# Optimization experiments

Hardware: AMD Instinct MI355X
Metric: run time of the kernel (lower is better)

The kernel has to match this reference:

```python
import jax, jax.numpy as jnp
import numpy as np

N_NODES = 100000
N_EDGES = 6400000
NUM_FEATURES = 128
NUM_CLASSES = 4


def _gcn_conv(x, W, b, src, dst, n):
    # PyG GCNConv: h = x @ W, symmetric norm over edges (self-loops already added),
    # scatter-add messages to dst, then add bias.
    h = x @ W                                            # [N, out]
    deg = jax.ops.segment_sum(jnp.ones(dst.shape[0], x.dtype), dst, num_segments=n)
    dinv = jnp.where(deg > 0, jax.lax.rsqrt(deg), 0.0)   # deg^-1/2, 0 for isolated
    norm = dinv[src] * dinv[dst]                         # [E]
    agg = jax.ops.segment_sum(h[src] * norm[:, None], dst, num_segments=n)
    return agg + b


def setup_inputs() -> dict:
    key = jax.random.key(0)
    ks = jax.random.split(key, 10)
    x = jax.random.normal(ks[0], (N_NODES, NUM_FEATURES), dtype=jnp.float32)
    edge_index = jax.random.randint(ks[1], (2, N_EDGES), 0, N_NODES, dtype=jnp.int32)

    def lin(k, fan_in, fan_out):
        s = 1.0 / np.sqrt(fan_in)
        return jax.random.uniform(k, (fan_in, fan_out), jnp.float32, -s, s)

    return {
        "x": x,
        "edge_index": edge_index,
        "W1": lin(ks[2], NUM_FEATURES, 4), "b1": jnp.zeros((4,), jnp.float32),
        "W2": lin(ks[3], 4, 4),            "b2": jnp.zeros((4,), jnp.float32),
        "W3": lin(ks[4], 4, 2),            "b3": jnp.zeros((2,), jnp.float32),
        "Wc": lin(ks[5], 2, NUM_CLASSES),  "bc": jnp.zeros((NUM_CLASSES,), jnp.float32),
    }


def reference(x, edge_index, W1, b1, W2, b2, W3, b3, Wc, bc):
    n = x.shape[0]
    loops = jnp.arange(n, dtype=edge_index.dtype)
    src = jnp.concatenate([edge_index[0], loops])  # add self-loops once; graph fixed across layers
    dst = jnp.concatenate([edge_index[1], loops])

    h = jnp.tanh(_gcn_conv(x, W1, b1, src, dst, n))
    h = jnp.tanh(_gcn_conv(h, W2, b2, src, dst, n))
    h = jnp.tanh(_gcn_conv(h, W3, b3, src, dst, n))
    out = h @ Wc + bc
    return (out, h)
```

## Files before the change

### kernel.cpp

```cpp
#include <hip/hip_runtime.h>
#include <math.h>


#define LCHUNK 16384
#define CHUNK2 16000
#define MAXNB  512
#define CAP    18432
#define MAXNB2 1024
#define CAP2   9600

__device__ __forceinline__ int swz_chunk(int bid, int G) {
    if ((G & 7) != 0) return bid;
    return (bid & 7) * (G >> 3) + (bid >> 3);
}

__global__ __launch_bounds__(1024) void k_local(
        const int* __restrict__ src, const int* __restrict__ dst,
        int* __restrict__ packed, int* __restrict__ hbT, int* __restrict__ loff,
        int NBK, int G, int e) {
    __shared__ int hist[MAXNB];
    __shared__ int cur[MAXNB];
    __shared__ int part[1024];
    __shared__ int stage[LCHUNK];
    int g = blockIdx.x, tid = threadIdx.x;
    for (int b = tid; b < NBK; b += 1024) hist[b] = 0;
    __syncthreads();
    int i0 = g * LCHUNK;
    int i1 = min(i0 + LCHUNK, e);
    int val[16], bkt[16];
#pragma unroll
    for (int k = 0; k < 16; k++) {
        int i = i0 + tid + (k << 10);
        bool v = i < i1;
        int d = v ? dst[i] : 0;
        int s = v ? src[i] : 0;
        bkt[k] = v ? (d >> 8) : -1;
        val[k] = ((d & 255) << 17) | s;
        if (v) atomicAdd(&hist[d >> 8], 1);
    }
    __syncthreads();
    int s0 = (tid < NBK) ? hist[tid] : 0;
    part[tid] = s0;
    __syncthreads();
#pragma unroll
    for (int off = 1; off < 1024; off <<= 1) {
        int u = (tid >= off) ? part[tid - off] : 0;
        __syncthreads();
        part[tid] += u;
        __syncthreads();
    }
    int excl = part[tid] - s0;
    if (tid < NBK) {
        cur[tid] = excl;
        hbT[(size_t)tid * G + g] = s0;
        loff[(size_t)g * NBK + tid] = excl;
    }
    __syncthreads();
#pragma unroll
    for (int k = 0; k < 16; k++) {
        if (bkt[k] >= 0) {
            int p = atomicAdd(&cur[bkt[k]], 1);
            stage[p] = val[k];
        }
    }
    __syncthreads();
    int len = i1 - i0;
    for (int i = tid; i < len; i += 1024)
        packed[i0 + i] = stage[i];
}

__global__ void k_scanA(int* __restrict__ hbT, int* __restrict__ btot, int G) {
    __shared__ int part[256];
    int b = blockIdx.x, t = threadIdx.x;
    int* row = hbT + (size_t)b * G;
    int C = (G + 255) / 256;
    int lo = t * C, hi = min(lo + C, G);
    int s = 0;
    for (int i = lo; i < hi; i++) s += row[i];
    part[t] = s;
    __syncthreads();
#pragma unroll
    for (int off = 1; off < 256; off <<= 1) {
        int u = (t >= off) ? part[t - off] : 0;
        __syncthreads();
        part[t] += u;
        __syncthreads();
    }
    int run = part[t] - s;
    for (int i = lo; i < hi; i++) {
        int v = row[i];
        row[i] = run;
        run += v;
    }
    if (t == 255) btot[b] = part[255];
}

__global__ void k_scanB(const int* __restrict__ btot, int* __restrict__ bstart,
                        int NB, int e) {
    __shared__ int part[512];
    int t = threadIdx.x;
    int C = (NB + 511) / 512;
    int lo = t * C, hi = min(lo + C, NB);
    int s = 0;
    for (int i = lo; i < hi; i++) s += btot[i];
    part[t] = s;
    __syncthreads();
#pragma unroll
    for (int off = 1; off < 512; off <<= 1) {
        int u = (t >= off) ? part[t - off] : 0;
        __syncthreads();
        part[t] += u;
        __syncthreads();
    }
    int run = part[t] - s;
    for (int i = lo; i < hi; i++) {
        bstart[i] = run;
        run += btot[i];
    }
    if (t == 511) bstart[NB] = e;
}

__global__ __launch_bounds__(512) void k_merge(
        const int* __restrict__ hbT, const int* __restrict__ loff,
        const int* __restrict__ btot, const int* __restrict__ bstart,
        const int* __restrict__ packed, int* __restrict__ csr,
        float* __restrict__ dinv, int* __restrict__ rowoff,
        int NBK, int G, int n) {
    __shared__ int stage[CAP];
    __shared__ int stage2[CAP];
    __shared__ int cnt[256];
    __shared__ int off[256];
    __shared__ int cur[256];
    int b = blockIdx.x, tid = threadIdx.x;
    int btt = btot[b];
    int total = min(btt, CAP);
    for (int g = tid; g < G; g += 512) {
        int o  = hbT[(size_t)b * G + g];
        int nx = (g + 1 < G) ? hbT[(size_t)b * G + g + 1] : btt;
        if (nx > CAP) nx = CAP;
        if (o >= nx) continue;
        int len = nx - o;
        int sp = g * LCHUNK + loff[(size_t)g * NBK + b];
        int a   = sp & ~3;
        int rel = sp - a;
        int n4  = (rel + len + 3) >> 2;
        for (int q = 0; q < n4; q++) {
            int4 w = *reinterpret_cast<const int4*>(packed + a + q * 4);
            int base = q * 4 - rel;
            if (base >= 0 && base < len)     stage[o + base]     = w.x;
            if (base + 1 >= 0 && base + 1 < len) stage[o + base + 1] = w.y;
            if (base + 2 >= 0 && base + 2 < len) stage[o + base + 2] = w.z;
            if (base + 3 >= 0 && base + 3 < len) stage[o + base + 3] = w.w;
        }
    }
    if (tid < 256) cnt[tid] = 0;
    __syncthreads();
    for (int i = tid; i < total; i += 512) atomicAdd(&cnt[stage[i] >> 17], 1);
    __syncthreads();
    if (tid < 256) off[tid] = cnt[tid];
    __syncthreads();
#pragma unroll
    for (int s = 1; s < 256; s <<= 1) {
        int v = 0;
        if (tid < 256 && tid >= s) v = off[tid - s];
        __syncthreads();
        if (tid < 256 && tid >= s) off[tid] += v;
        __syncthreads();
    }
    if (tid < 256) {
        int excl = off[tid] - cnt[tid];
        int node = (b << 8) + tid;
        if (node < n) dinv[node] = 1.0f / sqrtf((float)(cnt[tid] + 1));
        if (node <= n) rowoff[node] = bstart[b] + excl;
        cur[tid] = excl;
    }
    __syncthreads();
    for (int i = tid; i < total; i += 512) {
        int w = stage[i];
        int p = atomicAdd(&cur[w >> 17], 1);
        stage2[p] = w & 0x1FFFF;
    }
    __syncthreads();
    int base = bstart[b];
    for (int i = tid; i < total; i += 512)
        csr[base + i] = stage2[i];
}

__global__ void k_hist_o(const int* __restrict__ dst, int* __restrict__ hbT,
                         int NB, int G, int e) {
    __shared__ int hist[MAXNB2];
    int g = swz_chunk(blockIdx.x, G);
    for (int b = threadIdx.x; b < NB; b += 512) hist[b] = 0;
    __syncthreads();
    long long i0 = (long long)g * CHUNK2;
    int i1 = (int)min(i0 + CHUNK2, (long long)e);
    for (int i = (int)i0 + threadIdx.x; i < i1; i += 512)
        atomicAdd(&hist[dst[i] >> 7], 1);
    __syncthreads();
    for (int b = threadIdx.x; b < NB; b += 512)
        hbT[(size_t)b * G + g] = hist[b];
}

__global__ void k_part_o(const int* __restrict__ src, const int* __restrict__ dst,
                         const int* __restrict__ hbT, const int* __restrict__ bstart,
                         int* __restrict__ packed, int NB, int G, int e) {
    __shared__ int cur[MAXNB2];
    int g = swz_chunk(blockIdx.x, G);
    for (int b = threadIdx.x; b < NB; b += 512)
        cur[b] = hbT[(size_t)b * G + g] + bstart[b];
    __syncthreads();
    long long i0 = (long long)g * CHUNK2;
    int i1 = (int)min(i0 + CHUNK2, (long long)e);
    for (int i = (int)i0 + threadIdx.x; i < i1; i += 512) {
        int d = dst[i], s = src[i];
        int pos = atomicAdd(&cur[d >> 7], 1);
        packed[pos] = ((d & 127) << 17) | s;
    }
}

__global__ void k_build_o(const int* __restrict__ bstart, int* __restrict__ packed,
                          float* __restrict__ dinv, int* __restrict__ rowoff, int n) {
    __shared__ int stage[CAP2];
    __shared__ int cnt[128];
    __shared__ int off[128];
    __shared__ int cur[128];
    int b = blockIdx.x, tid = threadIdx.x;
    int lo = bstart[b];
    int len = bstart[b + 1] - lo;
    if (len > CAP2) len = CAP2;
    if (tid < 128) cnt[tid] = 0;
    for (int i = tid; i < len; i += 256) stage[i] = packed[lo + i];
    __syncthreads();
    for (int i = tid; i < len; i += 256) atomicAdd(&cnt[stage[i] >> 17], 1);
    __syncthreads();
    if (tid < 128) off[tid] = cnt[tid];
    __syncthreads();
#pragma unroll
    for (int s = 1; s < 128; s <<= 1) {
        int v = 0;
        if (tid < 128 && tid >= s) v = off[tid - s];
        __syncthreads();
        if (tid < 128 && tid >= s) off[tid] += v;
        __syncthreads();
    }
    if (tid < 128) {
        int excl = off[tid] - cnt[tid];
        int node = (b << 7) + tid;
        if (node < n) dinv[node] = 1.0f / sqrtf((float)(cnt[tid] + 1));
        if (node <= n) rowoff[node] = lo + excl;
        cur[tid] = excl;
    }
    __syncthreads();
    for (int i = tid; i < len; i += 256) {
        int w = stage[i];
        int p = atomicAdd(&cur[w >> 17], 1);
        packed[lo + p] = w & 0x1FFFF;
    }
}

__global__ void k_mm1(const float* __restrict__ x, const float* __restrict__ W,
                      const float* __restrict__ dinv, float* __restrict__ hs, int n) {
    int gid = blockIdx.x * blockDim.x + threadIdx.x;
    int node = gid >> 6;
    int lane = threadIdx.x & 63;
    if (node >= n) return;
    const float2 xv = *reinterpret_cast<const float2*>(x + (size_t)node * 128 + lane * 2);
    const float4 w0 = *reinterpret_cast<const float4*>(W + (lane * 2) * 4);
    const float4 w1 = *reinterpret_cast<const float4*>(W + (lane * 2 + 1) * 4);
    float a0 = xv.x * w0.x + xv.y * w1.x;
    float a1 = xv.x * w0.y + xv.y * w1.y;
    float a2 = xv.x * w0.z + xv.y * w1.z;
    float a3 = xv.x * w0.w + xv.y * w1.w;
#pragma unroll
    for (int m = 32; m >= 1; m >>= 1) {
        a0 += __shfl_xor(a0, m);
        a1 += __shfl_xor(a1, m);
        a2 += __shfl_xor(a2, m);
        a3 += __shfl_xor(a3, m);
    }
    if (lane == 0) {
        float di = dinv[node];
        *reinterpret_cast<float4*>(hs + (size_t)node * 4) =
            make_float4(a0 * di, a1 * di, a2 * di, a3 * di);
    }
}

template <int FOUT>
__global__ void k_gath_fin4(const int* __restrict__ rowoff, const int* __restrict__ csr,
                            const float* __restrict__ hs, const float* __restrict__ dinv,
                            const float* __restrict__ b, const float* __restrict__ Wn,
                            float* __restrict__ hsn, int n) {
    int gid = blockIdx.x * blockDim.x + threadIdx.x;
    int node = gid >> 6;
    int lane = threadIdx.x & 63;
    if (node >= n) return;
    int start = rowoff[node], end = rowoff[node + 1];
    float a0 = 0.f, a1 = 0.f, a2 = 0.f, a3 = 0.f;
    for (int j = start + lane; j < end; j += 64) {
        int s = csr[j];
        float4 v = *reinterpret_cast<const float4*>(hs + (size_t)s * 4);
        a0 += v.x; a1 += v.y; a2 += v.z; a3 += v.w;
    }
#pragma unroll
    for (int m = 32; m >= 1; m >>= 1) {
        a0 += __shfl_xor(a0, m);
        a1 += __shfl_xor(a1, m);
        a2 += __shfl_xor(a2, m);
        a3 += __shfl_xor(a3, m);
    }
    if (lane == 0) {
        float4 s = *reinterpret_cast<const float4*>(hs + (size_t)node * 4);
        float di = dinv[node];
        float h0 = tanhf((a0 + s.x) * di + b[0]);
        float h1 = tanhf((a1 + s.y) * di + b[1]);
        float h2 = tanhf((a2 + s.z) * di + b[2]);
        float h3 = tanhf((a3 + s.w) * di + b[3]);
        float o[FOUT];
#pragma unroll
        for (int j = 0; j < FOUT; j++) {
            o[j] = (h0 * Wn[0 * FOUT + j] + h1 * Wn[1 * FOUT + j] +
                    h2 * Wn[2 * FOUT + j] + h3 * Wn[3 * FOUT + j]) * di;
        }
        if constexpr (FOUT == 4) {
            *reinterpret_cast<float4*>(hsn + (size_t)node * 4) =
                make_float4(o[0], o[1], o[2], o[3]);
        } else {
            *reinterpret_cast<float2*>(hsn + (size_t)node * 2) = make_float2(o[0], o[1]);
        }
    }
}

__global__ void k_gath_fin3(const int* __restrict__ rowoff, const int* __restrict__ csr,
                            const float* __restrict__ hs, const float* __restrict__ dinv,
                            const float* __restrict__ b3, const float* __restrict__ Wc,
                            const float* __restrict__ bc, float* __restrict__ out,
                            float* __restrict__ hout, int n) {
    int gid = blockIdx.x * blockDim.x + threadIdx.x;
    int node = gid >> 6;
    int lane = threadIdx.x & 63;
    if (node >= n) return;
    int start = rowoff[node], end = rowoff[node + 1];
    float a0 = 0.f, a1 = 0.f;
    for (int j = start + lane; j < end; j += 64) {
        int s = csr[j];
        float2 v = *reinterpret_cast<const float2*>(hs + (size_t)s * 2);
        a0 += v.x; a1 += v.y;
    }
#pragma unroll
    for (int m = 32; m >= 1; m >>= 1) {
        a0 += __shfl_xor(a0, m);
        a1 += __shfl_xor(a1, m);
    }
    if (lane == 0) {
        float2 s = *reinterpret_cast<const float2*>(hs + (size_t)node * 2);
        float di = dinv[node];
        float h0 = tanhf((a0 + s.x) * di + b3[0]);
        float h1 = tanhf((a1 + s.y) * di + b3[1]);
        *reinterpret_cast<float2*>(hout + (size_t)node * 2) = make_float2(h0, h1);
        float4 o;
        o.x = h0 * Wc[0] + h1 * Wc[4] + bc[0];
        o.y = h0 * Wc[1] + h1 * Wc[5] + bc[1];
        o.z = h0 * Wc[2] + h1 * Wc[6] + bc[2];
        o.w = h0 * Wc[3] + h1 * Wc[7] + bc[3];
        *reinterpret_cast<float4*>(out + (size_t)node * 4) = o;
    }
}

extern "C" void kernel_launch(void* const* d_in, const int* in_sizes, int n_in,
                              void* d_out, int out_size, void* d_ws, size_t ws_size,
                              hipStream_t stream) {
    const float* x  = (const float*)d_in[0];
    const int*  ei  = (const int*)d_in[1];
    const float* W1 = (const float*)d_in[2];
    const float* b1 = (const float*)d_in[3];
    const float* W2 = (const float*)d_in[4];
    const float* b2 = (const float*)d_in[5];
    const float* W3 = (const float*)d_in[6];
    const float* b3 = (const float*)d_in[7];
    const float* Wc = (const float*)d_in[8];
    const float* bc = (const float*)d_in[9];

    const int n = in_sizes[0] / 128;
    const int e = in_sizes[1] / 2;
    const int* src = ei;
    const int* dst = ei + e;

    const size_t MB = 1024 * 1024;
    char* ws = (char*)d_ws;
    float* dinv   = (float*)(ws + 0);
    float* hsA    = (float*)(ws + MB / 2);
    float* hsB    = (float*)(ws + 2 * MB + MB / 2);
    int*   rowoff = (int*)  (ws + 4 * MB + MB / 2);
    int*   btot   = (int*)  (ws + 5 * MB);
    int*   bstart = (int*)  (ws + 5 * MB + 16 * 1024);
    int*   hbT    = (int*)  (ws + 5 * MB + MB / 2);
    int*   loff   = (int*)  (ws + 8 * MB);
    int*   packed = (int*)  (ws + 10 * MB + MB / 2);
    int*   csr    = (int*)  (ws + 36 * MB + MB / 2);

    float* out  = (float*)d_out;
    float* hout = out + (size_t)n * 4;

    const size_t need_new = 36 * MB + MB / 2 + (size_t)e * 4 + MB;
    const bool use_new = ws_size >= need_new;

    const int* csr_p;
    if (use_new) {
        const int NBK = (n + 255) >> 8;
        const int G = (e + LCHUNK - 1) / LCHUNK;
        k_local<<<G, 1024, 0, stream>>>(src, dst, packed, hbT, loff, NBK, G, e);
        k_scanA<<<NBK, 256, 0, stream>>>(hbT, btot, G);
        k_scanB<<<1, 512, 0, stream>>>(btot, bstart, NBK, e);
        k_merge<<<NBK, 512, 0, stream>>>(hbT, loff, btot, bstart, packed, csr,
                                         dinv, rowoff, NBK, G, n);
        csr_p = csr;
    } else {
        const int NB2 = (n + 127) >> 7;
        const int G2 = (e + CHUNK2 - 1) / CHUNK2;
        k_hist_o<<<G2, 512, 0, stream>>>(dst, hbT, NB2, G2, e);
        k_scanA<<<NB2, 256, 0, stream>>>(hbT, btot, G2);
        k_scanB<<<1, 512, 0, stream>>>(btot, bstart, NB2, e);
        k_part_o<<<G2, 512, 0, stream>>>(src, dst, hbT, bstart, packed, NB2, G2, e);
        k_build_o<<<NB2, 256, 0, stream>>>(bstart, packed, dinv, rowoff, n);
        csr_p = packed;
    }

    const int wb = (n + 3) / 4;
    k_mm1<<<wb, 256, 0, stream>>>(x, W1, dinv, hsA, n);

    k_gath_fin4<4><<<wb, 256, 0, stream>>>(rowoff, csr_p, hsA, dinv, b1, W2, hsB, n);
    k_gath_fin4<2><<<wb, 256, 0, stream>>>(rowoff, csr_p, hsB, dinv, b2, W3, hsA, n);
    k_gath_fin3<<<wb, 256, 0, stream>>>(rowoff, csr_p, hsA, dinv, b3, Wc, bc, out, hout, n);

    (void)n_in; (void)out_size;
}
```

Measured before the change: 218.0 us.

## Use 16-lane groups per node for gathers and split finalize into separate kernels

The gather kernels now assign 16 threads per node instead of a full 64-lane wavefront, since the average degree is around 64 and many lanes would otherwise idle. Each gather writes raw aggregates to a new workspace buffer. Separate per-node kernels then apply the tanh, bias and next-layer matmul, so that work no longer runs on a single lane per wavefront. This adds three kernel launches and an extra round trip through global memory for the aggregate buffer, and the workspace layout is shifted to make room for it.

```diff
diff --git a/kernel.cpp b/kernel.cpp
--- a/kernel.cpp
+++ b/kernel.cpp
@@ -285,85 +285,98 @@
     }
 }
 
-template <int FOUT>
-__global__ void k_gath_fin4(const int* __restrict__ rowoff, const int* __restrict__ csr,
-                            const float* __restrict__ hs, const float* __restrict__ dinv,
-                            const float* __restrict__ b, const float* __restrict__ Wn,
-                            float* __restrict__ hsn, int n) {
+__global__ void k_gath4(const int* __restrict__ rowoff, const int* __restrict__ csr,
+                        const float* __restrict__ hs, float* __restrict__ agg, int n) {
     int gid = blockIdx.x * blockDim.x + threadIdx.x;
-    int node = gid >> 6;
-    int lane = threadIdx.x & 63;
+    int node = gid >> 4;
+    int sub = threadIdx.x & 15;
     if (node >= n) return;
     int start = rowoff[node], end = rowoff[node + 1];
     float a0 = 0.f, a1 = 0.f, a2 = 0.f, a3 = 0.f;
-    for (int j = start + lane; j < end; j += 64) {
+    for (int j = start + sub; j < end; j += 16) {
         int s = csr[j];
         float4 v = *reinterpret_cast<const float4*>(hs + (size_t)s * 4);
         a0 += v.x; a1 += v.y; a2 += v.z; a3 += v.w;
     }
 #pragma unroll
-    for (int m = 32; m >= 1; m >>= 1) {
+    for (int m = 8; m >= 1; m >>= 1) {
         a0 += __shfl_xor(a0, m);
         a1 += __shfl_xor(a1, m);
         a2 += __shfl_xor(a2, m);
         a3 += __shfl_xor(a3, m);
     }
-    if (lane == 0) {
-        float4 s = *reinterpret_cast<const float4*>(hs + (size_t)node * 4);
-        float di = dinv[node];
-        float h0 = tanhf((a0 + s.x) * di + b[0]);
-        float h1 = tanhf((a1 + s.y) * di + b[1]);
-        float h2 = tanhf((a2 + s.z) * di + b[2]);
-        float h3 = tanhf((a3 + s.w) * di + b[3]);
-        float o[FOUT];
-#pragma unroll
-        for (int j = 0; j < FOUT; j++) {
-            o[j] = (h0 * Wn[0 * FOUT + j] + h1 * Wn[1 * FOUT + j] +
-                    h2 * Wn[2 * FOUT + j] + h3 * Wn[3 * FOUT + j]) * di;
-        }
-        if constexpr (FOUT == 4) {
-            *reinterpret_cast<float4*>(hsn + (size_t)node * 4) =
-                make_float4(o[0], o[1], o[2], o[3]);
-        } else {
-            *reinterpret_cast<float2*>(hsn + (size_t)node * 2) = make_float2(o[0], o[1]);
-        }
-    }
-}
-
-__global__ void k_gath_fin3(const int* __restrict__ rowoff, const int* __restrict__ csr,
-                            const float* __restrict__ hs, const float* __restrict__ dinv,
-                            const float* __restrict__ b3, const float* __restrict__ Wc,
-                            const float* __restrict__ bc, float* __restrict__ out,
-                            float* __restrict__ hout, int n) {
+    if (sub == 0)
+        *reinterpret_cast<float4*>(agg + (size_t)node * 4) =
+            make_float4(a0, a1, a2, a3);
+}
+
+__global__ void k_gath2(const int* __restrict__ rowoff, const int* __restrict__ csr,
+                        const float* __restrict__ hs, float* __restrict__ agg, int n) {
     int gid = blockIdx.x * blockDim.x + threadIdx.x;
-    int node = gid >> 6;
-    int lane = threadIdx.x & 63;
+    int node = gid >> 4;
+    int sub = threadIdx.x & 15;
     if (node >= n) return;
     int start = rowoff[node], end = rowoff[node + 1];
     float a0 = 0.f, a1 = 0.f;
-    for (int j = start + lane; j < end; j += 64) {
+    for (int j = start + sub; j < end; j += 16) {
         int s = csr[j];
         float2 v = *reinterpret_cast<const float2*>(hs + (size_t)s * 2);
         a0 += v.x; a1 += v.y;
     }
 #pragma unroll
-    for (int m = 32; m >= 1; m >>= 1) {
+    for (int m = 8; m >= 1; m >>= 1) {
         a0 += __shfl_xor(a0, m);
         a1 += __shfl_xor(a1, m);
     }
-    if (lane == 0) {
-        float2 s = *reinterpret_cast<const float2*>(hs + (size_t)node * 2);
-        float di = dinv[node];
-        float h0 = tanhf((a0 + s.x) * di + b3[0]);
-        float h1 = tanhf((a1 + s.y) * di + b3[1]);
-        *reinterpret_cast<float2*>(hout + (size_t)node * 2) = make_float2(h0, h1);
-        float4 o;
-        o.x = h0 * Wc[0] + h1 * Wc[4] + bc[0];
-        o.y = h0 * Wc[1] + h1 * Wc[5] + bc[1];
-        o.z = h0 * Wc[2] + h1 * Wc[6] + bc[2];
-        o.w = h0 * Wc[3] + h1 * Wc[7] + bc[3];
-        *reinterpret_cast<float4*>(out + (size_t)node * 4) = o;
-    }
+    if (sub == 0)
+        *reinterpret_cast<float2*>(agg + (size_t)node * 2) = make_float2(a0, a1);
+}
+
+template <int FOUT>
+__global__ void k_fin4(const float* __restrict__ agg, const float* __restrict__ hs,
+                       const float* __restrict__ dinv, const float* __restrict__ b_,
+                       const float* __restrict__ Wn, float* __restrict__ hsn, int n) {
+    int i = blockIdx.x * blockDim.x + threadIdx.x;
+    if (i >= n) return;
+    float4 a = *reinterpret_cast<const float4*>(agg + (size_t)i * 4);
+    float4 s = *reinterpret_cast<const float4*>(hs + (size_t)i * 4);
+    float di = dinv[i];
+    float h0 = tanhf((a.x + s.x) * di + b_[0]);
+    float h1 = tanhf((a.y + s.y) * di + b_[1]);
+    float h2 = tanhf((a.z + s.z) * di + b_[2]);
+    float h3 = tanhf((a.w + s.w) * di + b_[3]);
+    float o[FOUT];
+#pragma unroll
+    for (int j = 0; j < FOUT; j++) {
+        o[j] = (h0 * Wn[0 * FOUT + j] + h1 * Wn[1 * FOUT + j] +
+                h2 * Wn[2 * FOUT + j] + h3 * Wn[3 * FOUT + j]) * di;
+    }
+    if constexpr (FOUT == 4) {
+        *reinterpret_cast<float4*>(hsn + (size_t)i * 4) =
+            make_float4(o[0], o[1], o[2], o[3]);
+    } else {
+        *reinterpret_cast<float2*>(hsn + (size_t)i * 2) = make_float2(o[0], o[1]);
+    }
+}
+
+__global__ void k_fin3(const float* __restrict__ agg, const float* __restrict__ hs,
+                       const float* __restrict__ dinv, const float* __restrict__ b3,
+                       const float* __restrict__ Wc, const float* __restrict__ bc,
+                       float* __restrict__ out, float* __restrict__ hout, int n) {
+    int i = blockIdx.x * blockDim.x + threadIdx.x;
+    if (i >= n) return;
+    float2 a = *reinterpret_cast<const float2*>(agg + (size_t)i * 2);
+    float2 s = *reinterpret_cast<const float2*>(hs + (size_t)i * 2);
+    float di = dinv[i];
+    float h0 = tanhf((a.x + s.x) * di + b3[0]);
+    float h1 = tanhf((a.y + s.y) * di + b3[1]);
+    *reinterpret_cast<float2*>(hout + (size_t)i * 2) = make_float2(h0, h1);
+    float4 o;
+    o.x = h0 * Wc[0] + h1 * Wc[4] + bc[0];
+    o.y = h0 * Wc[1] + h1 * Wc[5] + bc[1];
+    o.z = h0 * Wc[2] + h1 * Wc[6] + bc[2];
+    o.w = h0 * Wc[3] + h1 * Wc[7] + bc[3];
+    *reinterpret_cast<float4*>(out + (size_t)i * 4) = o;
 }
 
 extern "C" void kernel_launch(void* const* d_in, const int* in_sizes, int n_in,
@@ -394,14 +407,15 @@
     int*   btot   = (int*)  (ws + 5 * MB);
     int*   bstart = (int*)  (ws + 5 * MB + 16 * 1024);
     int*   hbT    = (int*)  (ws + 5 * MB + MB / 2);
-    int*   loff   = (int*)  (ws + 8 * MB);
-    int*   packed = (int*)  (ws + 10 * MB + MB / 2);
-    int*   csr    = (int*)  (ws + 36 * MB + MB / 2);
+    float* agg    = (float*)(ws + 8 * MB);
+    int*   loff   = (int*)  (ws + 10 * MB);
+    int*   packed = (int*)  (ws + 12 * MB);
+    int*   csr    = (int*)  (ws + 38 * MB);
 
     float* out  = (float*)d_out;
     float* hout = out + (size_t)n * 4;
 
-    const size_t need_new = 36 * MB + MB / 2 + (size_t)e * 4 + MB;
+    const size_t need_new = 38 * MB + (size_t)e * 4 + MB;
     const bool use_new = ws_size >= need_new;
 
     const int* csr_p;
@@ -426,11 +440,16 @@
     }
 
     const int wb = (n + 3) / 4;
+    const int qb = (n + 15) / 16;
+    const int nb = (n + 255) / 256;
     k_mm1<<<wb, 256, 0, stream>>>(x, W1, dinv, hsA, n);
 
-    k_gath_fin4<4><<<wb, 256, 0, stream>>>(rowoff, csr_p, hsA, dinv, b1, W2, hsB, n);
-    k_gath_fin4<2><<<wb, 256, 0, stream>>>(rowoff, csr_p, hsB, dinv, b2, W3, hsA, n);
-    k_gath_fin3<<<wb, 256, 0, stream>>>(rowoff, csr_p, hsA, dinv, b3, Wc, bc, out, hout, n);
+    k_gath4<<<qb, 256, 0, stream>>>(rowoff, csr_p, hsA, agg, n);
+    k_fin4<4><<<nb, 256, 0, stream>>>(agg, hsA, dinv, b1, W2, hsB, n);
+    k_gath4<<<qb, 256, 0, stream>>>(rowoff, csr_p, hsB, agg, n);
+    k_fin4<2><<<nb, 256, 0, stream>>>(agg, hsB, dinv, b2, W3, hsA, n);
+    k_gath2<<<qb, 256, 0, stream>>>(rowoff, csr_p, hsA, agg, n);
+    k_fin3<<<nb, 256, 0, stream>>>(agg, hsA, dinv, b3, Wc, bc, out, hout, n);
 
     (void)n_in; (void)out_size;
 }
```

Result: faster. 201.4 us (median of 2 runs) (-7.6%).
